# Performance work log

Measured on AMD Instinct MI355X. Metric: run time of the kernel, lower is better.

The kernel has to match this reference:

```python
import jax, jax.numpy as jnp
import numpy as np

B, S, E, H = 4, 2048, 1024, 16
D = E // H  # head_dim


def setup_inputs() -> dict:
    key = jax.random.key(0)
    ks = jax.random.split(key, 7)
    scale = 1.0 / np.sqrt(E)
    return {
        "query": jax.random.normal(ks[0], (B, S, E), dtype=jnp.float32),
        "key": jax.random.normal(ks[1], (B, S, E), dtype=jnp.float32),
        "value": jax.random.normal(ks[2], (B, S, E), dtype=jnp.float32),
        "Wq": jax.random.normal(ks[3], (E, E), dtype=jnp.float32) * scale,
        "Wk": jax.random.normal(ks[4], (E, E), dtype=jnp.float32) * scale,
        "Wv": jax.random.normal(ks[5], (E, E), dtype=jnp.float32) * scale,
        "Wo": jax.random.normal(ks[6], (E, E), dtype=jnp.float32) * scale,
    }


def reference(query, key, value, Wq, Wk, Wv, Wo):
    b, s, e = query.shape
    sm_scale = (e // H) ** -0.5
    # TTLinear: x @ W.T; reshape to [b, h, s, d]
    q = (query @ Wq.T).reshape(b, s, H, D).transpose(0, 2, 1, 3)
    k = (key @ Wk.T).reshape(b, s, H, D).transpose(0, 2, 1, 3)
    v = (value @ Wv.T).reshape(b, s, H, D).transpose(0, 2, 1, 3)
    scores = jnp.einsum("bhqd,bhkd->bhqk", q, k) * sm_scale  # [b,h,s,s]
    attn = jax.nn.softmax(scores, axis=-1)
    out = jnp.einsum("bhqk,bhkd->bhqd", attn, v)
    out = out.transpose(0, 2, 1, 3).reshape(b, s, e)
    # dropout is identity in eval mode
    return out @ Wo.T
```

## Files before the change

kernel.cpp:

```cpp
#include <hip/hip_runtime.h>
#include <hip/hip_bf16.h>

#define BB 4
#define SS 2048
#define EE 1024
#define HH 16
#define DD 64
#define MM (BB*SS)

using f16x8 = __attribute__((ext_vector_type(8))) _Float16;
using f16x4 = __attribute__((ext_vector_type(4))) _Float16;
using f32x4 = __attribute__((ext_vector_type(4))) float;
using f32x16 = __attribute__((ext_vector_type(16))) float;

typedef __attribute__((address_space(3))) void       as3_void;
typedef const __attribute__((address_space(1))) void as1_cvoid;

__device__ __forceinline__ void async16(void* lds, const void* g) {
    __builtin_amdgcn_global_load_lds((as1_cvoid*)g, (as3_void*)lds, 16, 0, 0);
}

__device__ __forceinline__ f16x8 cvt8(const float* src) {
    const float4 v0 = *(const float4*)src;
    const float4 v1 = *(const float4*)(src + 4);
    f16x8 h;
    h[0] = (_Float16)v0.x; h[1] = (_Float16)v0.y;
    h[2] = (_Float16)v0.z; h[3] = (_Float16)v0.w;
    h[4] = (_Float16)v1.x; h[5] = (_Float16)v1.y;
    h[6] = (_Float16)v1.z; h[7] = (_Float16)v1.w;
    return h;
}

__global__ __launch_bounds__(256) void cvt_all(const float* __restrict__ q,
                                               const float* __restrict__ k,
                                               const float* __restrict__ v,
                                               const float* __restrict__ w0,
                                               const float* __restrict__ w1,
                                               const float* __restrict__ w2,
                                               const float* __restrict__ w3,
                                               _Float16* __restrict__ dq,
                                               _Float16* __restrict__ dk,
                                               _Float16* __restrict__ dv,
                                               _Float16* __restrict__ wf,
                                               int aN8, int wN8) {
    int seg = blockIdx.y;
    int i = blockIdx.x * 256 + threadIdx.x;
    const float* s; _Float16* d; int n8;
    if (seg < 3) {
        s = seg == 0 ? q : seg == 1 ? k : v;
        d = seg == 0 ? dq : seg == 1 ? dk : dv;
        n8 = aN8;
    } else {
        int t = seg - 3;
        s = t == 0 ? w0 : t == 1 ? w1 : t == 2 ? w2 : w3;
        d = wf + (size_t)t * EE * EE;
        n8 = wN8;
    }
    if (i < n8) ((f16x8*)d)[i] = cvt8(s + (size_t)i * 8);
}

__device__ __forceinline__ void swizzle512(int fid, int& m0, int& n0) {
    int xcd  = fid & 7;
    int s    = fid >> 3;
    int band = xcd + 8 * (s >> 5);
    int w    = s & 31;
    m0 = (band * 4 + (w & 3)) * 128;
    n0 = (w >> 2) * 128;
}

__global__ __launch_bounds__(256) void gemm_qkv(const _Float16* __restrict__ A0,
                                                const _Float16* __restrict__ A1,
                                                const _Float16* __restrict__ A2,
                                                const _Float16* __restrict__ W,
                                                _Float16* __restrict__ Cb,
                                                int M, int N, int K) {
    constexpr int BM = 128, BN = 128, BK = 64;
    __shared__ alignas(16) _Float16 As[2][BM * 32];
    __shared__ alignas(16) _Float16 Bs[2][BN * 32];

    const int tid  = threadIdx.x;
    const int lane = tid & 63;
    const int wave = tid >> 6;
    const int wm   = (wave >> 1) * 64;
    const int wn   = (wave & 1) * 64;
    const int quad = lane >> 4;
    const int c    = lane & 15;
    int m0, n0;
    swizzle512(blockIdx.x, m0, n0);
    const int z = blockIdx.y;

    const _Float16* A  = z == 0 ? A0 : z == 1 ? A1 : A2;
    const _Float16* Bw = W + (size_t)z * EE * EE;
    _Float16* C = Cb + (size_t)z * MM * EE;
    const float osc = (z == 0) ? 0.18033688f : 1.0f;

    f32x4 acc[4][4] = {};

    for (int k0 = 0; k0 < K; k0 += BK) {
#pragma unroll
        for (int p = 0; p < 4; ++p) {
            int half = p >> 1;
            int remb = (p & 1) * 256 + wave * 64;
            int rem  = remb + lane;
            int row  = rem >> 2, kc = (rem & 3) * 8;
            async16(&As[half][remb * 8], A  + (size_t)(m0 + row) * K + k0 + half * 32 + kc);
            async16(&Bs[half][remb * 8], Bw + (size_t)(n0 + row) * K + k0 + half * 32 + kc);
        }
        __syncthreads();

#pragma unroll
        for (int ks = 0; ks < 2; ++ks) {
            f16x8 af[4], bf[4];
#pragma unroll
            for (int i = 0; i < 4; ++i)
                af[i] = *(const f16x8*)&As[ks][(wm + i * 16 + c) * 32 + quad * 8];
#pragma unroll
            for (int j = 0; j < 4; ++j)
                bf[j] = *(const f16x8*)&Bs[ks][(wn + j * 16 + c) * 32 + quad * 8];
#pragma unroll
            for (int i = 0; i < 4; ++i)
#pragma unroll
                for (int j = 0; j < 4; ++j)
                    acc[i][j] = __builtin_amdgcn_mfma_f32_16x16x32_f16(af[i], bf[j], acc[i][j], 0, 0, 0);
        }
        __syncthreads();
    }

#pragma unroll
    for (int i = 0; i < 4; ++i)
#pragma unroll
        for (int j = 0; j < 4; ++j)
#pragma unroll
            for (int r = 0; r < 4; ++r) {
                int row = m0 + wm + i * 16 + quad * 4 + r;
                int col = n0 + wn + j * 16 + c;
                C[(size_t)row * N + col] = (_Float16)(acc[i][j][r] * osc);
            }
}

__global__ __launch_bounds__(256) void gemm_wo(const _Float16* __restrict__ A,
                                               const _Float16* __restrict__ Bw,
                                               float* __restrict__ C,
                                               int M, int N, int K) {
    constexpr int BM = 128, BN = 128, BK = 64;
    __shared__ alignas(16) _Float16 As[2][BM * 32];
    __shared__ alignas(16) _Float16 Bs[2][BN * 32];

    const int tid  = threadIdx.x;
    const int lane = tid & 63;
    const int wave = tid >> 6;
    const int wm   = (wave >> 1) * 64;
    const int wn   = (wave & 1) * 64;
    const int quad = lane >> 4;
    const int c    = lane & 15;
    int m0, n0;
    swizzle512(blockIdx.x, m0, n0);

    f32x4 acc[4][4] = {};

    for (int k0 = 0; k0 < K; k0 += BK) {
#pragma unroll
        for (int p = 0; p < 4; ++p) {
            int half = p >> 1;
            int remb = (p & 1) * 256 + wave * 64;
            int rem  = remb + lane;
            int row  = rem >> 2, kc = (rem & 3) * 8;
            async16(&As[half][remb * 8], A  + (size_t)(m0 + row) * K + k0 + half * 32 + kc);
            async16(&Bs[half][remb * 8], Bw + (size_t)(n0 + row) * K + k0 + half * 32 + kc);
        }
        __syncthreads();

#pragma unroll
        for (int ks = 0; ks < 2; ++ks) {
            f16x8 af[4], bf[4];
#pragma unroll
            for (int i = 0; i < 4; ++i)
                af[i] = *(const f16x8*)&As[ks][(wm + i * 16 + c) * 32 + quad * 8];
#pragma unroll
            for (int j = 0; j < 4; ++j)
                bf[j] = *(const f16x8*)&Bs[ks][(wn + j * 16 + c) * 32 + quad * 8];
#pragma unroll
            for (int i = 0; i < 4; ++i)
#pragma unroll
                for (int j = 0; j < 4; ++j)
                    acc[i][j] = __builtin_amdgcn_mfma_f32_16x16x32_f16(af[i], bf[j], acc[i][j], 0, 0, 0);
        }
        __syncthreads();
    }

#pragma unroll
    for (int i = 0; i < 4; ++i)
#pragma unroll
        for (int j = 0; j < 4; ++j)
#pragma unroll
            for (int r = 0; r < 4; ++r) {
                int row = m0 + wm + i * 16 + quad * 4 + r;
                int col = n0 + wn + j * 16 + c;
                C[(size_t)row * N + col] = acc[i][j][r];
            }
}

__global__ __launch_bounds__(256, 3) void attn_kernel(const _Float16* __restrict__ Q,
                                                      const _Float16* __restrict__ K,
                                                      const _Float16* __restrict__ V,
                                                      _Float16* __restrict__ O) {
    constexpr int NT = SS / 64;
    __shared__ alignas(16) _Float16 Ks[2][8 * 512];
    __shared__ alignas(16) _Float16 Vf[2][8 * 512];

    const int tid  = threadIdx.x;
    const int lane = tid & 63;
    const int wave = tid >> 6;
    const int l31  = lane & 31;
    const int hl   = lane >> 5;
    const int bh   = blockIdx.x;
    const int b    = bh >> 4, h = bh & 15;
    const int q0   = blockIdx.y * 128;

    const _Float16* Qg = Q + (size_t)(b * SS + q0) * EE + h * DD;
    const _Float16* Kg = K + (size_t)(b * SS) * EE + h * DD;
    const _Float16* Vg = V + (size_t)(b * SS) * EE + h * DD;

    f16x8 qf[4];
#pragma unroll
    for (int ks = 0; ks < 4; ++ks)
        qf[ks] = *(const f16x8*)(Qg + (size_t)(wave * 32 + l31) * EE + ks * 16 + hl * 8);

    f16x8 vreg[2];

#pragma unroll
    for (int p = 0; p < 2; ++p) {
        int f = wave * 2 + p;
        int kvt = f >> 2, ks = f & 3;
        async16(&Ks[0][f * 512],
                Kg + (size_t)(kvt * 32 + l31) * EE + ks * 16 + hl * 8);
    }
#pragma unroll
    for (int p = 0; p < 2; ++p) {
        int ch = tid + p * 256;
        int d = ch & 63, scg = ch >> 6;
        f16x8 hv;
#pragma unroll
        for (int j = 0; j < 8; ++j) hv[j] = Vg[(size_t)(scg * 8 + j) * EE + d];
        vreg[p] = hv;
    }
    __syncthreads();

    float lsum = 0.f;
    f32x16 o0 = {}, o1 = {};

    for (int t = 0; t < NT; ++t) {
        const int buf = t & 1;
        const int s1 = (t + 1) * 64;

        if (t + 1 < NT) {
#pragma unroll
            for (int p = 0; p < 2; ++p) {
                int f = wave * 2 + p;
                int kvt = f >> 2, ks = f & 3;
                async16(&Ks[buf ^ 1][f * 512],
                        Kg + (size_t)(s1 + kvt * 32 + l31) * EE + ks * 16 + hl * 8);
            }
        }
#pragma unroll
        for (int p = 0; p < 2; ++p) {
            int ch = tid + p * 256;
            int d = ch & 63, scg = ch >> 6;
            int g  = (scg >> 1) * 2 + (d >> 5);
            int lp = (d & 31) + 32 * (scg & 1);
            *(f16x8*)&Vf[buf][g * 512 + lp * 8] = vreg[p];
        }

        f16x8 pB[4];
#pragma unroll
        for (int kvt = 0; kvt < 2; ++kvt) {
            f32x16 s = {};
            __builtin_amdgcn_s_setprio(1);
#pragma unroll
            for (int ks = 0; ks < 4; ++ks) {
                f16x8 af = *(const f16x8*)&Ks[buf][(kvt * 4 + ks) * 512 + lane * 8];
                s = __builtin_amdgcn_mfma_f32_32x32x16_f16(af, qf[ks], s, 0, 0, 0);
            }
            __builtin_amdgcn_s_setprio(0);
            float p[16];
#pragma unroll
            for (int r = 0; r < 16; ++r) {
                p[r] = __builtin_amdgcn_exp2f(s[r]);
                lsum += p[r];
            }
            int w[8];
#pragma unroll
            for (int i = 0; i < 8; ++i)
                w[i] = __builtin_bit_cast(int, __builtin_amdgcn_cvt_pkrtz(p[2 * i], p[2 * i + 1]));
            asm("v_permlane32_swap_b32 %0, %1" : "+v"(w[0]), "+v"(w[2]));
            asm("v_permlane32_swap_b32 %0, %1" : "+v"(w[1]), "+v"(w[3]));
            asm("v_permlane32_swap_b32 %0, %1" : "+v"(w[4]), "+v"(w[6]));
            asm("v_permlane32_swap_b32 %0, %1" : "+v"(w[5]), "+v"(w[7]));
            int4 lo; lo.x = w[0]; lo.y = w[1]; lo.z = w[2]; lo.w = w[3];
            int4 hi; hi.x = w[4]; hi.y = w[5]; hi.z = w[6]; hi.w = w[7];
            pB[kvt * 2 + 0] = __builtin_bit_cast(f16x8, lo);
            pB[kvt * 2 + 1] = __builtin_bit_cast(f16x8, hi);
        }

        __syncthreads();

        if (t + 1 < NT) {
#pragma unroll
            for (int p = 0; p < 2; ++p) {
                int ch = tid + p * 256;
                int d = ch & 63, scg = ch >> 6;
                f16x8 hv;
#pragma unroll
                for (int j = 0; j < 8; ++j) hv[j] = Vg[(size_t)(s1 + scg * 8 + j) * EE + d];
                vreg[p] = hv;
            }
        }

        __builtin_amdgcn_s_setprio(1);
#pragma unroll
        for (int ks = 0; ks < 4; ++ks) {
            f16x8 v0 = *(const f16x8*)&Vf[buf][(ks * 2 + 0) * 512 + lane * 8];
            o0 = __builtin_amdgcn_mfma_f32_32x32x16_f16(v0, pB[ks], o0, 0, 0, 0);
            f16x8 v1 = *(const f16x8*)&Vf[buf][(ks * 2 + 1) * 512 + lane * 8];
            o1 = __builtin_amdgcn_mfma_f32_32x32x16_f16(v1, pB[ks], o1, 0, 0, 0);
        }
        __builtin_amdgcn_s_setprio(0);
    }

    float lt  = lsum + __shfl_xor(lsum, 32);
    float inv = 1.0f / lt;
    _Float16* Og = O + (size_t)(b * SS + q0 + wave * 32 + l31) * EE + h * DD;
#pragma unroll
    for (int dt = 0; dt < 2; ++dt)
#pragma unroll
        for (int g = 0; g < 4; ++g) {
            f16x4 ov;
#pragma unroll
            for (int r = 0; r < 4; ++r) {
                float val = (dt == 0) ? o0[g * 4 + r] : o1[g * 4 + r];
                ov[r] = (_Float16)(val * inv);
            }
            *(f16x4*)&Og[dt * 32 + g * 8 + hl * 4] = ov;
        }
}

extern "C" void kernel_launch(void* const* d_in, const int* in_sizes, int n_in,
                              void* d_out, int out_size, void* d_ws, size_t ws_size,
                              hipStream_t stream) {
    const float* query = (const float*)d_in[0];
    const float* key   = (const float*)d_in[1];
    const float* value = (const float*)d_in[2];
    const float* Wq    = (const float*)d_in[3];
    const float* Wk    = (const float*)d_in[4];
    const float* Wv    = (const float*)d_in[5];
    const float* Wo    = (const float*)d_in[6];
    float* out = (float*)d_out;

    const size_t NE = (size_t)MM * EE;
    const size_t NW = (size_t)EE * EE;
    _Float16* Qw   = (_Float16*)d_ws;
    _Float16* Kw   = Qw + NE;
    _Float16* Vw   = Kw + NE;
    _Float16* Wf   = Vw + NE;
    _Float16* Qact = Wf + 4 * NW;
    _Float16* Kact = (_Float16*)d_out;
    _Float16* Vact = Kact + NE;

    dim3 blk(256);
    const int wN8 = (int)(NW / 8), aN8 = (int)(NE / 8);

    cvt_all<<<dim3(aN8 / 256, 7), blk, 0, stream>>>(query, key, value, Wq, Wk, Wv, Wo,
                                                    Qact, Kact, Vact, Wf, aN8, wN8);

    gemm_qkv<<<dim3(512, 3), blk, 0, stream>>>(Qact, Kact, Vact, Wf, Qw, MM, EE, EE);

    attn_kernel<<<dim3(BB * HH, SS / 128), blk, 0, stream>>>(Qw, Kw, Vw, Qact);

    gemm_wo<<<dim3(512), blk, 0, stream>>>(Qact, Wf + 3 * NW, out, MM, EE, EE);
}
```

Before: 337.9 us.

## Write V transposed from projection GEMM and async-load it in attention

The QKV projection epilogue now writes V (z==2) in a per-head transposed [b,h,d,s] layout with vectorized f16x4 stores. The attention kernel then loads V tiles with async global-to-LDS copies instead of strided scalar gathers through registers and a separate LDS scatter. This removes one barrier per iteration, interleaves the PV MFMAs with each half's softmax, and raises launch bounds occupancy to 4. The transposed store is uncoalesced in the GEMM epilogue, and the higher occupancy target may pressure registers. The V path also skips the osc scaling, which is correct only if osc is 1 for V.

```diff
diff --git a/kernel.cpp b/kernel.cpp
--- a/kernel.cpp
+++ b/kernel.cpp
@@ -126,16 +126,31 @@
         __syncthreads();
     }
 
-#pragma unroll
-    for (int i = 0; i < 4; ++i)
-#pragma unroll
-        for (int j = 0; j < 4; ++j)
-#pragma unroll
-            for (int r = 0; r < 4; ++r) {
-                int row = m0 + wm + i * 16 + quad * 4 + r;
-                int col = n0 + wn + j * 16 + c;
-                C[(size_t)row * N + col] = (_Float16)(acc[i][j][r] * osc);
-            }
+    if (z == 2) {
+#pragma unroll
+        for (int i = 0; i < 4; ++i)
+#pragma unroll
+            for (int j = 0; j < 4; ++j) {
+                int col  = n0 + wn + j * 16 + c;
+                int rowb = m0 + wm + i * 16 + quad * 4;
+                int bq = rowb >> 11, sI = rowb & 2047;
+                f16x4 ov;
+#pragma unroll
+                for (int r = 0; r < 4; ++r) ov[r] = (_Float16)acc[i][j][r];
+                *(f16x4*)&C[(((size_t)bq * HH + (col >> 6)) * DD + (col & 63)) * SS + sI] = ov;
+            }
+    } else {
+#pragma unroll
+        for (int i = 0; i < 4; ++i)
+#pragma unroll
+            for (int j = 0; j < 4; ++j)
+#pragma unroll
+                for (int r = 0; r < 4; ++r) {
+                    int row = m0 + wm + i * 16 + quad * 4 + r;
+                    int col = n0 + wn + j * 16 + c;
+                    C[(size_t)row * N + col] = (_Float16)(acc[i][j][r] * osc);
+                }
+    }
 }
 
 __global__ __launch_bounds__(256) void gemm_wo(const _Float16* __restrict__ A,
@@ -200,13 +215,13 @@
             }
 }
 
-__global__ __launch_bounds__(256, 3) void attn_kernel(const _Float16* __restrict__ Q,
+__global__ __launch_bounds__(256, 4) void attn_kernel(const _Float16* __restrict__ Q,
                                                       const _Float16* __restrict__ K,
-                                                      const _Float16* __restrict__ V,
+                                                      const _Float16* __restrict__ Vt,
                                                       _Float16* __restrict__ O) {
     constexpr int NT = SS / 64;
     __shared__ alignas(16) _Float16 Ks[2][8 * 512];
-    __shared__ alignas(16) _Float16 Vf[2][8 * 512];
+    __shared__ alignas(16) _Float16 Vs[2][8 * 512];
 
     const int tid  = threadIdx.x;
     const int lane = tid & 63;
@@ -217,32 +232,31 @@
     const int b    = bh >> 4, h = bh & 15;
     const int q0   = blockIdx.y * 128;
 
-    const _Float16* Qg = Q + (size_t)(b * SS + q0) * EE + h * DD;
-    const _Float16* Kg = K + (size_t)(b * SS) * EE + h * DD;
-    const _Float16* Vg = V + (size_t)(b * SS) * EE + h * DD;
+    const _Float16* Qg  = Q  + (size_t)(b * SS + q0) * EE + h * DD;
+    const _Float16* Kg  = K  + (size_t)(b * SS) * EE + h * DD;
+    const _Float16* Vtg = Vt + (size_t)bh * DD * SS;
 
     f16x8 qf[4];
 #pragma unroll
     for (int ks = 0; ks < 4; ++ks)
         qf[ks] = *(const f16x8*)(Qg + (size_t)(wave * 32 + l31) * EE + ks * 16 + hl * 8);
 
-    f16x8 vreg[2];
-
+    const _Float16* kp[2];
+    const _Float16* vp[2];
 #pragma unroll
     for (int p = 0; p < 2; ++p) {
         int f = wave * 2 + p;
-        int kvt = f >> 2, ks = f & 3;
-        async16(&Ks[0][f * 512],
-                Kg + (size_t)(kvt * 32 + l31) * EE + ks * 16 + hl * 8);
-    }
+        int kvt = f >> 2, ksk = f & 3;
+        kp[p] = Kg + (size_t)(kvt * 32 + l31) * EE + ksk * 16 + hl * 8;
+        int ksv = f >> 1, dt = f & 1;
+        vp[p] = Vtg + (size_t)(dt * 32 + l31) * SS + ksv * 16 + hl * 8;
+    }
+
 #pragma unroll
     for (int p = 0; p < 2; ++p) {
-        int ch = tid + p * 256;
-        int d = ch & 63, scg = ch >> 6;
-        f16x8 hv;
-#pragma unroll
-        for (int j = 0; j < 8; ++j) hv[j] = Vg[(size_t)(scg * 8 + j) * EE + d];
-        vreg[p] = hv;
+        int f = wave * 2 + p;
+        async16(&Ks[0][f * 512], kp[p]);
+        async16(&Vs[0][f * 512], vp[p]);
     }
     __syncthreads();
 
@@ -251,37 +265,36 @@
 
     for (int t = 0; t < NT; ++t) {
         const int buf = t & 1;
-        const int s1 = (t + 1) * 64;
 
         if (t + 1 < NT) {
 #pragma unroll
             for (int p = 0; p < 2; ++p) {
                 int f = wave * 2 + p;
-                int kvt = f >> 2, ks = f & 3;
-                async16(&Ks[buf ^ 1][f * 512],
-                        Kg + (size_t)(s1 + kvt * 32 + l31) * EE + ks * 16 + hl * 8);
-            }
-        }
-#pragma unroll
-        for (int p = 0; p < 2; ++p) {
-            int ch = tid + p * 256;
-            int d = ch & 63, scg = ch >> 6;
-            int g  = (scg >> 1) * 2 + (d >> 5);
-            int lp = (d & 31) + 32 * (scg & 1);
-            *(f16x8*)&Vf[buf][g * 512 + lp * 8] = vreg[p];
-        }
+                kp[p] += 64 * EE;
+                vp[p] += 64;
+                async16(&Ks[buf ^ 1][f * 512], kp[p]);
+                async16(&Vs[buf ^ 1][f * 512], vp[p]);
+            }
+        }
+
+        f32x16 sa = {}, sb = {};
+        __builtin_amdgcn_s_setprio(1);
+#pragma unroll
+        for (int ks = 0; ks < 4; ++ks) {
+            f16x8 af = *(const f16x8*)&Ks[buf][ks * 512 + lane * 8];
+            sa = __builtin_amdgcn_mfma_f32_32x32x16_f16(af, qf[ks], sa, 0, 0, 0);
+        }
+#pragma unroll
+        for (int ks = 0; ks < 4; ++ks) {
+            f16x8 af = *(const f16x8*)&Ks[buf][(4 + ks) * 512 + lane * 8];
+            sb = __builtin_amdgcn_mfma_f32_32x32x16_f16(af, qf[ks], sb, 0, 0, 0);
+        }
+        __builtin_amdgcn_s_setprio(0);
 
         f16x8 pB[4];
 #pragma unroll
         for (int kvt = 0; kvt < 2; ++kvt) {
-            f32x16 s = {};
-            __builtin_amdgcn_s_setprio(1);
-#pragma unroll
-            for (int ks = 0; ks < 4; ++ks) {
-                f16x8 af = *(const f16x8*)&Ks[buf][(kvt * 4 + ks) * 512 + lane * 8];
-                s = __builtin_amdgcn_mfma_f32_32x32x16_f16(af, qf[ks], s, 0, 0, 0);
-            }
-            __builtin_amdgcn_s_setprio(0);
+            const f32x16& s = kvt ? sb : sa;
             float p[16];
 #pragma unroll
             for (int r = 0; r < 16; ++r) {
@@ -300,31 +313,19 @@
             int4 hi; hi.x = w[4]; hi.y = w[5]; hi.z = w[6]; hi.w = w[7];
             pB[kvt * 2 + 0] = __builtin_bit_cast(f16x8, lo);
             pB[kvt * 2 + 1] = __builtin_bit_cast(f16x8, hi);
-        }
-
-        __syncthreads();
-
-        if (t + 1 < NT) {
-#pragma unroll
-            for (int p = 0; p < 2; ++p) {
-                int ch = tid + p * 256;
-                int d = ch & 63, scg = ch >> 6;
-                f16x8 hv;
-#pragma unroll
-                for (int j = 0; j < 8; ++j) hv[j] = Vg[(size_t)(s1 + scg * 8 + j) * EE + d];
-                vreg[p] = hv;
-            }
-        }
-
-        __builtin_amdgcn_s_setprio(1);
-#pragma unroll
-        for (int ks = 0; ks < 4; ++ks) {
-            f16x8 v0 = *(const f16x8*)&Vf[buf][(ks * 2 + 0) * 512 + lane * 8];
-            o0 = __builtin_amdgcn_mfma_f32_32x32x16_f16(v0, pB[ks], o0, 0, 0, 0);
-            f16x8 v1 = *(const f16x8*)&Vf[buf][(ks * 2 + 1) * 512 + lane * 8];
-            o1 = __builtin_amdgcn_mfma_f32_32x32x16_f16(v1, pB[ks], o1, 0, 0, 0);
-        }
-        __builtin_amdgcn_s_setprio(0);
+
+            __builtin_amdgcn_s_setprio(1);
+#pragma unroll
+            for (int ks = kvt * 2; ks < kvt * 2 + 2; ++ks) {
+                f16x8 v0 = *(const f16x8*)&Vs[buf][(ks * 2 + 0) * 512 + lane * 8];
+                o0 = __builtin_amdgcn_mfma_f32_32x32x16_f16(v0, pB[ks], o0, 0, 0, 0);
+                f16x8 v1 = *(const f16x8*)&Vs[buf][(ks * 2 + 1) * 512 + lane * 8];
+                o1 = __builtin_amdgcn_mfma_f32_32x32x16_f16(v1, pB[ks], o1, 0, 0, 0);
+            }
+            __builtin_amdgcn_s_setprio(0);
+        }
+
+        __syncthreads();
     }
 
     float lt  = lsum + __shfl_xor(lsum, 32);
```

Measured after the change: 340.0 us. About the same (+0.6%).
